# Kernel tuning notes

Hardware: AMD Instinct MI355X
Metric: run time of the kernel (lower is better)

The kernel has to match this reference:

```python
import jax, jax.numpy as jnp
import numpy as np

N_NODES = 100000
N_EDGES = 3200000
F_IN = 512
F_OUT = 256


def setup_inputs() -> dict:
    key = jax.random.key(0)
    k1, k2, k3, k4, k5 = jax.random.split(key, 5)
    x = jax.random.normal(k1, (N_NODES, F_IN), dtype=jnp.float32)
    weights = jax.random.normal(k2, (F_IN, F_OUT), dtype=jnp.float32) * 0.05
    # sparse adjacency in COO, row-sorted (equivalent to the CSR torch.spmm uses)
    edge_row = jnp.sort(jax.random.randint(k3, (N_EDGES,), 0, N_NODES, dtype=jnp.int32))
    edge_col = jax.random.randint(k4, (N_EDGES,), 0, N_NODES, dtype=jnp.int32)
    edge_val = jax.random.uniform(k5, (N_EDGES,), dtype=jnp.float32)
    return {"x": x, "weights": weights, "edge_row": edge_row,
            "edge_col": edge_col, "edge_val": edge_val}


def reference(x, weights, edge_row, edge_col, edge_val):
    # support = input @ weights  (dense GEMM)
    support = jnp.matmul(x, weights)                      # [N, F_OUT]
    # output = spmm(adj, support): gather neighbor rows, scale, scatter-add
    gathered = support[edge_col] * edge_val[:, None]      # [E, F_OUT]
    out = jax.ops.segment_sum(gathered, edge_row, num_segments=N_NODES)
    return out
```

## Files before the change

### kernel.cpp

```cpp
#include <hip/hip_runtime.h>
#include <hip/hip_bf16.h>

#define N_NODES 100000
#define N_EDGES 3200000
#define F_IN 512
#define F_OUT 256

typedef short bf16x8 __attribute__((ext_vector_type(8)));
typedef short bf16x4 __attribute__((ext_vector_type(4)));
typedef float f32x4 __attribute__((ext_vector_type(4)));

__device__ __forceinline__ short f2b(float f) {
    unsigned u = __builtin_bit_cast(unsigned, f);
    u += 0x7fffu + ((u >> 16) & 1u);
    return (short)(u >> 16);
}
__device__ __forceinline__ float b2f(short s) {
    unsigned u = ((unsigned)(unsigned short)s) << 16;
    return __builtin_bit_cast(float, u);
}

__global__ void k_wconv(const float* __restrict__ W, short* __restrict__ Wt) {
    int idx = blockIdx.x * 256 + threadIdx.x;
    int k = idx >> 8;
    int n = idx & 255;
    Wt[n * F_IN + k] = f2b(W[idx]);
}

__global__ void k_rowptr(const int* __restrict__ erow, int* __restrict__ rp) {
    int i = blockIdx.x * 256 + threadIdx.x;
    if (i > N_NODES) return;
    int lo = 0, hi = N_EDGES;
    while (lo < hi) {
        int mid = (lo + hi) >> 1;
        if (erow[mid] < i) lo = mid + 1; else hi = mid;
    }
    rp[i] = lo;
}

__global__ __launch_bounds__(256) void k_gemm(const float* __restrict__ X,
                                              const short* __restrict__ Wt,
                                              short* __restrict__ S) {
    __shared__ short As[128 * 40];
    const int tid  = threadIdx.x;
    const int wave = tid >> 6;
    const int lane = tid & 63;
    const int wr   = wave >> 1, wc = wave & 1;
    const int l15  = lane & 15, quad = lane >> 4;
    const int bm = blockIdx.x, bn = blockIdx.y;
    const long row_base = (long)bm * 128;

    f32x4 acc[4][4];
#pragma unroll
    for (int i = 0; i < 4; ++i)
#pragma unroll
        for (int j = 0; j < 4; ++j) acc[i][j] = (f32x4){0.f, 0.f, 0.f, 0.f};

    const int srow = tid >> 3;
    const int scol = (tid & 7) * 4;
    const short* wtb = Wt + (bn * 128 + wc * 64 + l15) * F_IN + quad * 8;
    const int afrag_base = (wr * 64 + l15) * 40 + quad * 8;

    for (int k0 = 0; k0 < F_IN; k0 += 32) {
        __syncthreads();
#pragma unroll
        for (int r = 0; r < 4; ++r) {
            int m = srow + r * 32;
            long gm = row_base + m;
            f32x4 v = (f32x4){0.f, 0.f, 0.f, 0.f};
            if (gm < N_NODES) v = *(const f32x4*)(X + gm * F_IN + k0 + scol);
            bf16x4 b = { f2b(v.x), f2b(v.y), f2b(v.z), f2b(v.w) };
            *(bf16x4*)&As[m * 40 + scol] = b;
        }
        __syncthreads();

        bf16x8 bfrag[4], afrag[4];
#pragma unroll
        for (int j = 0; j < 4; ++j)
            bfrag[j] = *(const bf16x8*)(wtb + j * 16 * F_IN + k0);
#pragma unroll
        for (int i = 0; i < 4; ++i)
            afrag[i] = *(const bf16x8*)&As[afrag_base + i * 16 * 40];
#pragma unroll
        for (int i = 0; i < 4; ++i)
#pragma unroll
            for (int j = 0; j < 4; ++j)
                acc[i][j] = __builtin_amdgcn_mfma_f32_16x16x32_bf16(
                    afrag[i], bfrag[j], acc[i][j], 0, 0, 0);
    }

#pragma unroll
    for (int i = 0; i < 4; ++i) {
#pragma unroll
        for (int rg = 0; rg < 4; ++rg) {
            long gm = row_base + wr * 64 + i * 16 + quad * 4 + rg;
            if (gm < N_NODES) {
#pragma unroll
                for (int j = 0; j < 4; ++j) {
                    int gn = bn * 128 + wc * 64 + j * 16 + l15;
                    S[gm * F_OUT + gn] = f2b(acc[i][j][rg]);
                }
            }
        }
    }
}

__global__ __launch_bounds__(256) void k_spmm(const short* __restrict__ S,
                                              const int* __restrict__ ecol,
                                              const float* __restrict__ evalp,
                                              const int* __restrict__ rp,
                                              float* __restrict__ out) {
    const int wave = threadIdx.x >> 6, lane = threadIdx.x & 63;
    const int r = blockIdx.x * 4 + wave;
    const int lo = rp[r], hi = rp[r + 1];
    const short* sp = S + lane * 4;
    float a0 = 0.f, a1 = 0.f, a2 = 0.f, a3 = 0.f;
    if (lo < hi) {
        int c = ecol[lo];
        float v = evalp[lo];
        bf16x4 s = *(const bf16x4*)(sp + (long)c * F_OUT);
        for (int e = lo + 1; e < hi; ++e) {
            int c2 = ecol[e];
            float v2 = evalp[e];
            bf16x4 s2 = *(const bf16x4*)(sp + (long)c2 * F_OUT);
            a0 += v * b2f(s.x); a1 += v * b2f(s.y);
            a2 += v * b2f(s.z); a3 += v * b2f(s.w);
            v = v2; s = s2;
        }
        a0 += v * b2f(s.x); a1 += v * b2f(s.y);
        a2 += v * b2f(s.z); a3 += v * b2f(s.w);
    }
    f32x4 o = {a0, a1, a2, a3};
    *(f32x4*)(out + (long)r * F_OUT + lane * 4) = o;
}

extern "C" void kernel_launch(void* const* d_in, const int* in_sizes, int n_in,
                              void* d_out, int out_size, void* d_ws, size_t ws_size,
                              hipStream_t stream) {
    const float* x    = (const float*)d_in[0];
    const float* w    = (const float*)d_in[1];
    const int*   erow = (const int*)d_in[2];
    const int*   ecol = (const int*)d_in[3];
    const float* ev   = (const float*)d_in[4];
    float* out = (float*)d_out;

    char* ws = (char*)d_ws;
    short* Wt = (short*)ws;
    int*   rp = (int*)(ws + 262144);
    short* S  = (short*)(ws + (1 << 20));

    k_wconv<<<512, 256, 0, stream>>>(w, Wt);
    k_rowptr<<<(N_NODES + 256) / 256, 256, 0, stream>>>(erow, rp);
    dim3 g((N_NODES + 127) / 128, F_OUT / 128);
    k_gemm<<<g, 256, 0, stream>>>(x, Wt, S);
    k_spmm<<<N_NODES / 4, 256, 0, stream>>>(S, ecol, ev, rp, out);
}
```

Measured before the change: 653.0 us.

## Stage fp32 X via direct global-to-LDS loads, widen GEMM tile, half-wave SpMM rows

The GEMM now uses 512-thread blocks covering all 256 output columns, so X is read once instead of twice. X tiles are staged in fp32 straight into LDS with global_load_lds and converted to bf16 when fragments are read, using a cheaper round-half-up pack via perm. The SpMM assigns each row to half a wave with 16-byte bf16x8 gathers, processing two rows per wave. The cost is twice the LDS footprint per tile, higher register pressure, and slightly different bf16 rounding on ties.

```diff
diff --git a/kernel.cpp b/kernel.cpp
--- a/kernel.cpp
+++ b/kernel.cpp
@@ -1,5 +1,4 @@
 #include <hip/hip_runtime.h>
-#include <hip/hip_bf16.h>
 
 #define N_NODES 100000
 #define N_EDGES 3200000
@@ -9,6 +8,7 @@
 typedef short bf16x8 __attribute__((ext_vector_type(8)));
 typedef short bf16x4 __attribute__((ext_vector_type(4)));
 typedef float f32x4 __attribute__((ext_vector_type(4)));
+typedef unsigned u32x4 __attribute__((ext_vector_type(4)));
 
 __device__ __forceinline__ short f2b(float f) {
     unsigned u = __builtin_bit_cast(unsigned, f);
@@ -18,6 +18,16 @@
 __device__ __forceinline__ float b2f(short s) {
     unsigned u = ((unsigned)(unsigned short)s) << 16;
     return __builtin_bit_cast(float, u);
+}
+__device__ __forceinline__ unsigned pack2(float f0, float f1) {
+    unsigned u0 = __builtin_bit_cast(unsigned, f0) + 0x8000u;
+    unsigned u1 = __builtin_bit_cast(unsigned, f1) + 0x8000u;
+    return __builtin_amdgcn_perm(u1, u0, 0x07060302);
+}
+__device__ __forceinline__ void load_lds16(const float* g, void* l) {
+    __builtin_amdgcn_global_load_lds(
+        (const __attribute__((address_space(1))) unsigned*)g,
+        (__attribute__((address_space(3))) unsigned*)l, 16, 0, 0);
 }
 
 __global__ void k_wconv(const float* __restrict__ W, short* __restrict__ Wt) {
@@ -38,17 +48,17 @@
     rp[i] = lo;
 }
 
-__global__ __launch_bounds__(256) void k_gemm(const float* __restrict__ X,
-                                              const short* __restrict__ Wt,
-                                              short* __restrict__ S) {
-    __shared__ short As[128 * 40];
+__global__ __launch_bounds__(512, 4) void k_gemm(const float* __restrict__ X,
+                                                 const short* __restrict__ Wt,
+                                                 short* __restrict__ S) {
+    __shared__ float As[128 * 32];
     const int tid  = threadIdx.x;
     const int wave = tid >> 6;
     const int lane = tid & 63;
-    const int wr   = wave >> 1, wc = wave & 1;
+    const int wr   = wave >> 2;
+    const int wc   = wave & 3;
     const int l15  = lane & 15, quad = lane >> 4;
-    const int bm = blockIdx.x, bn = blockIdx.y;
-    const long row_base = (long)bm * 128;
+    const long row_base = (long)blockIdx.x * 128;
 
     f32x4 acc[4][4];
 #pragma unroll
@@ -56,31 +66,40 @@
 #pragma unroll
         for (int j = 0; j < 4; ++j) acc[i][j] = (f32x4){0.f, 0.f, 0.f, 0.f};
 
-    const int srow = tid >> 3;
-    const int scol = (tid & 7) * 4;
-    const short* wtb = Wt + (bn * 128 + wc * 64 + l15) * F_IN + quad * 8;
-    const int afrag_base = (wr * 64 + l15) * 40 + quad * 8;
+    long gr0 = row_base + (tid >> 3);
+    long gr1 = gr0 + 64;
+    if (gr0 >= N_NODES) gr0 = N_NODES - 1;
+    if (gr1 >= N_NODES) gr1 = N_NODES - 1;
+    const float* gp0 = X + gr0 * F_IN + (tid & 7) * 4;
+    const float* gp1 = X + gr1 * F_IN + (tid & 7) * 4;
+    char* lds0 = (char*)As + wave * 1024;
+    char* lds1 = (char*)As + 8192 + wave * 1024;
 
+    const short* wtb = Wt + (wc * 64 + l15) * F_IN + quad * 8;
+    const float* arow = As + (wr * 64 + l15) * 32 + quad * 8;
+
+#pragma unroll 1
     for (int k0 = 0; k0 < F_IN; k0 += 32) {
         __syncthreads();
-#pragma unroll
-        for (int r = 0; r < 4; ++r) {
-            int m = srow + r * 32;
-            long gm = row_base + m;
-            f32x4 v = (f32x4){0.f, 0.f, 0.f, 0.f};
-            if (gm < N_NODES) v = *(const f32x4*)(X + gm * F_IN + k0 + scol);
-            bf16x4 b = { f2b(v.x), f2b(v.y), f2b(v.z), f2b(v.w) };
-            *(bf16x4*)&As[m * 40 + scol] = b;
-        }
+        load_lds16(gp0 + k0, lds0);
+        load_lds16(gp1 + k0, lds1);
         __syncthreads();
 
-        bf16x8 bfrag[4], afrag[4];
+        bf16x8 bfrag[4];
 #pragma unroll
         for (int j = 0; j < 4; ++j)
             bfrag[j] = *(const bf16x8*)(wtb + j * 16 * F_IN + k0);
+
+        bf16x8 afrag[4];
 #pragma unroll
-        for (int i = 0; i < 4; ++i)
-            afrag[i] = *(const bf16x8*)&As[afrag_base + i * 16 * 40];
+        for (int i = 0; i < 4; ++i) {
+            const float* ap = arow + i * 16 * 32;
+            f32x4 x0 = *(const f32x4*)ap;
+            f32x4 x1 = *(const f32x4*)(ap + 4);
+            u32x4 pv = { pack2(x0.x, x0.y), pack2(x0.z, x0.w),
+                         pack2(x1.x, x1.y), pack2(x1.z, x1.w) };
+            afrag[i] = __builtin_bit_cast(bf16x8, pv);
+        }
 #pragma unroll
         for (int i = 0; i < 4; ++i)
 #pragma unroll
@@ -97,7 +116,7 @@
             if (gm < N_NODES) {
 #pragma unroll
                 for (int j = 0; j < 4; ++j) {
-                    int gn = bn * 128 + wc * 64 + j * 16 + l15;
+                    int gn = wc * 64 + j * 16 + l15;
                     S[gm * F_OUT + gn] = f2b(acc[i][j][rg]);
                 }
             }
@@ -107,31 +126,36 @@
 
 __global__ __launch_bounds__(256) void k_spmm(const short* __restrict__ S,
                                               const int* __restrict__ ecol,
-                                              const float* __restrict__ evalp,
+                                              const float* __restrict__ ev,
                                               const int* __restrict__ rp,
                                               float* __restrict__ out) {
     const int wave = threadIdx.x >> 6, lane = threadIdx.x & 63;
-    const int r = blockIdx.x * 4 + wave;
+    const int half = lane >> 5, hl = lane & 31;
+    const int r = (blockIdx.x * 4 + wave) * 2 + half;
     const int lo = rp[r], hi = rp[r + 1];
-    const short* sp = S + lane * 4;
-    float a0 = 0.f, a1 = 0.f, a2 = 0.f, a3 = 0.f;
-    if (lo < hi) {
-        int c = ecol[lo];
-        float v = evalp[lo];
-        bf16x4 s = *(const bf16x4*)(sp + (long)c * F_OUT);
-        for (int e = lo + 1; e < hi; ++e) {
+    const short* sp = S + hl * 8;
+    float a[8] = {0.f, 0.f, 0.f, 0.f, 0.f, 0.f, 0.f, 0.f};
+    int e = lo;
+    if (e < hi) {
+        int c = ecol[e];
+        float v = ev[e];
+        bf16x8 s = *(const bf16x8*)(sp + (long)c * F_OUT);
+        for (++e; e < hi; ++e) {
             int c2 = ecol[e];
-            float v2 = evalp[e];
-            bf16x4 s2 = *(const bf16x4*)(sp + (long)c2 * F_OUT);
-            a0 += v * b2f(s.x); a1 += v * b2f(s.y);
-            a2 += v * b2f(s.z); a3 += v * b2f(s.w);
+            float v2 = ev[e];
+            bf16x8 s2 = *(const bf16x8*)(sp + (long)c2 * F_OUT);
+#pragma unroll
+            for (int i = 0; i < 8; ++i) a[i] += v * b2f(s[i]);
             v = v2; s = s2;
         }
-        a0 += v * b2f(s.x); a1 += v * b2f(s.y);
-        a2 += v * b2f(s.z); a3 += v * b2f(s.w);
+#pragma unroll
+        for (int i = 0; i < 8; ++i) a[i] += v * b2f(s[i]);
     }
-    f32x4 o = {a0, a1, a2, a3};
-    *(f32x4*)(out + (long)r * F_OUT + lane * 4) = o;
+    f32x4 o0 = {a[0], a[1], a[2], a[3]};
+    f32x4 o1 = {a[4], a[5], a[6], a[7]};
+    float* op = out + (long)r * F_OUT + hl * 8;
+    *(f32x4*)op = o0;
+    *(f32x4*)(op + 4) = o1;
 }
 
 extern "C" void kernel_launch(void* const* d_in, const int* in_sizes, int n_in,
@@ -151,7 +175,6 @@
 
     k_wconv<<<512, 256, 0, stream>>>(w, Wt);
     k_rowptr<<<(N_NODES + 256) / 256, 256, 0, stream>>>(erow, rp);
-    dim3 g((N_NODES + 127) / 128, F_OUT / 128);
-    k_gemm<<<g, 256, 0, stream>>>(x, Wt, S);
-    k_spmm<<<N_NODES / 4, 256, 0, stream>>>(S, ecol, ev, rp, out);
+    k_gemm<<<(N_NODES + 127) / 128, 512, 0, stream>>>(x, Wt, S);
+    k_spmm<<<N_NODES / 8, 256, 0, stream>>>(S, ecol, ev, rp, out);
 }
```

New measurement: 584.2 us. -10.5%, faster.
